# Kernel tuning notes

Hardware: AMD Instinct MI355X
Metric: run time of the kernel (lower is better)

## Reference

```python
import jax, jax.numpy as jnp
import numpy as np

B, HRES, WRES, C, HEADS, WS, SS = 32, 64, 64, 256, 8, 8, 4
N = WS * WS
HID = 4 * C
EPS = 1e-5


def _rel_pos_index(ws):
    coords = np.stack(np.meshgrid(np.arange(ws), np.arange(ws), indexing='ij'))  # [2,ws,ws]
    cf = coords.reshape(2, -1)
    rel = (cf[:, :, None] - cf[:, None, :]).transpose(1, 2, 0)  # [N,N,2]
    rel[:, :, 0] += ws - 1
    rel[:, :, 1] += ws - 1
    rel[:, :, 0] *= 2 * ws - 1
    return rel.sum(-1).reshape(-1)  # [N*N]


def _attn_mask(H, W, ws, ss):
    img = np.zeros((H, W))
    cnt = 0
    for hs in (slice(0, -ws), slice(-ws, -ss), slice(-ss, None)):
        for wsl in (slice(0, -ws), slice(-ws, -ss), slice(-ss, None)):
            img[hs, wsl] = cnt
            cnt += 1
    mw = img.reshape(H // ws, ws, W // ws, ws).transpose(0, 2, 1, 3).reshape(-1, ws * ws)
    am = mw[:, None, :] - mw[:, :, None]  # [nW,N,N]
    return np.where(am != 0, -100.0, 0.0).astype(np.float32)


_RPI = jnp.asarray(_rel_pos_index(WS))
_MASK = jnp.asarray(_attn_mask(HRES, WRES, WS, SS))  # [nW,N,N]


def _ln(x, g, b):
    m = x.mean(-1, keepdims=True)
    v = ((x - m) ** 2).mean(-1, keepdims=True)
    return (x - m) / jnp.sqrt(v + EPS) * g + b


def setup_inputs() -> dict:
    key = jax.random.key(0)
    ks = jax.random.split(key, 16)
    s = 0.02
    return {
        'x': jax.random.normal(ks[0], (B, HRES * WRES, C), jnp.float32),
        'norm1_g': jnp.ones((C,), jnp.float32),
        'norm1_b': jnp.zeros((C,), jnp.float32),
        'qkv_w': jax.random.normal(ks[1], (3 * C, C), jnp.float32) * s,
        'qkv_b': jnp.zeros((3 * C,), jnp.float32),
        'rpb_table': jax.random.normal(ks[2], ((2 * WS - 1) ** 2, HEADS), jnp.float32) * s,
        'proj_w': jax.random.normal(ks[3], (C, C), jnp.float32) * s,
        'proj_b': jnp.zeros((C,), jnp.float32),
        'norm2_g': jnp.ones((C,), jnp.float32),
        'norm2_b': jnp.zeros((C,), jnp.float32),
        'fc1_w': jax.random.normal(ks[4], (HID, C), jnp.float32) * s,
        'fc1_b': jnp.zeros((HID,), jnp.float32),
        'fc2_w': jax.random.normal(ks[5], (C, HID), jnp.float32) * s,
        'fc2_b': jnp.zeros((C,), jnp.float32),
        'H': HRES,
        'W': WRES,
    }


def reference(x, norm1_g, norm1_b, qkv_w, qkv_b, rpb_table, proj_w, proj_b,
              norm2_g, norm2_b, fc1_w, fc1_b, fc2_w, fc2_b, H, W):
    Bn, L, Cd = x.shape
    ws, ss, nh = WS, SS, HEADS
    hd = Cd // nh
    shortcut = x
    h = _ln(x, norm1_g, norm1_b).reshape(Bn, H, W, Cd)
    # cyclic shift (H,W divisible by ws -> no padding needed)
    h = jnp.roll(h, (-ss, -ss), axis=(1, 2))
    # window partition: [B,H,W,C] -> [B*nW, N, C]
    h = h.reshape(Bn, H // ws, ws, W // ws, ws, Cd).transpose(0, 1, 3, 2, 4, 5).reshape(-1, N, Cd)
    qkv = (h @ qkv_w.T + qkv_b).reshape(-1, N, 3, nh, hd).transpose(2, 0, 3, 1, 4)
    q, k, v = qkv[0], qkv[1], qkv[2]  # [B_,h,N,d]
    attn = jnp.einsum('bhnd,bhmd->bhnm', q * (hd ** -0.5), k)
    rpb = rpb_table[_RPI].reshape(N, N, nh).transpose(2, 0, 1)  # [h,N,N]
    attn = attn + rpb[None]
    nW = _MASK.shape[0]
    attn = attn.reshape(Bn, nW, nh, N, N) + _MASK[None, :, None]
    attn = jax.nn.softmax(attn.reshape(-1, nh, N, N), axis=-1)
    o = jnp.einsum('bhnm,bhmd->bhnd', attn, v).transpose(0, 2, 1, 3).reshape(-1, N, Cd)
    o = o @ proj_w.T + proj_b
    # window reverse + reverse shift
    o = o.reshape(Bn, H // ws, W // ws, ws, ws, Cd).transpose(0, 1, 3, 2, 4, 5).reshape(Bn, H, W, Cd)
    o = jnp.roll(o, (ss, ss), axis=(1, 2)).reshape(Bn, L, Cd)
    x = shortcut + o
    h2 = _ln(x, norm2_g, norm2_b)
    h2 = jax.nn.gelu(h2 @ fc1_w.T + fc1_b, approximate=False)
    return x + (h2 @ fc2_w.T + fc2_b)
```

## Files before the change

kernel.cpp:

```cpp
#include <hip/hip_runtime.h>
#include <hip/hip_bf16.h>
#include <stdint.h>

typedef __bf16 bf16_t;
typedef __bf16 bf16x8 __attribute__((ext_vector_type(8)));
typedef __bf16 bf16x4 __attribute__((ext_vector_type(4)));
typedef float f32x4 __attribute__((ext_vector_type(4)));

#define MROWS 131072

__device__ __forceinline__ bf16_t to_bf16(float f) {
  __hip_bfloat16 h = __float2bfloat16(f);
  return *reinterpret_cast<bf16_t*>(&h);
}

__device__ __forceinline__ f32x4 mfma16(bf16x8 a, bf16x8 b, f32x4 c) {
  return __builtin_amdgcn_mfma_f32_16x16x32_bf16(a, b, c, 0, 0, 0);
}

__device__ __forceinline__ void gload16(const void* g, void* l) {
  __builtin_amdgcn_global_load_lds(
      (const __attribute__((address_space(1))) void*)g,
      (__attribute__((address_space(3))) void*)l, 16, 0, 0);
}

__device__ __forceinline__ int map_row(int m) {
  int b   = m >> 12;
  int rem = m & 4095;
  int win = rem >> 6;
  int n   = rem & 63;
  int gh  = ((win >> 3) << 3) + (n >> 3);
  int gw  = ((win & 7) << 3) + (n & 7);
  int sh  = (gh + 4) & 63;
  int sw  = (gw + 4) & 63;
  return (b << 12) + (sh << 6) + sw;
}

__global__ __launch_bounds__(256) void cvt_all(const float* __restrict__ qkv_w,
                                               const float* __restrict__ proj_w,
                                               const float* __restrict__ fc1_w,
                                               const float* __restrict__ fc2_w,
                                               bf16_t* __restrict__ qkv_o,
                                               bf16_t* __restrict__ proj_o,
                                               bf16_t* __restrict__ fc1_o,
                                               bf16_t* __restrict__ fc2_o) {
  int i = blockIdx.x * 256 + threadIdx.x;
  if (i < 196608)       qkv_o[i] = to_bf16(qkv_w[i]);
  else if (i < 262144)  proj_o[i - 196608] = to_bf16(proj_w[i - 196608]);
  else if (i < 524288)  fc1_o[i - 262144] = to_bf16(fc1_w[i - 262144]);
  else                  fc2_o[i - 524288] = to_bf16(fc2_w[i - 524288]);
}

__global__ __launch_bounds__(256) void bias_kernel(const float* __restrict__ rpbt,
                                                   float* __restrict__ bias) {
  int idx = blockIdx.x * 256 + threadIdx.x;
  int m = idx & 63, n = (idx >> 6) & 63, h = (idx >> 12) & 7, c = idx >> 15;
  int yn = n >> 3, xn = n & 7, ym = m >> 3, xm = m & 7;
  float v = rpbt[((yn - ym + 7) * 15 + (xn - xm + 7)) * 8 + h];
  int rn = (c & 2) ? (yn < 4 ? 1 : 2) : 0;
  int cn = (c & 1) ? (xn < 4 ? 1 : 2) : 0;
  int rm = (c & 2) ? (ym < 4 ? 1 : 2) : 0;
  int cm = (c & 1) ? (xm < 4 ? 1 : 2) : 0;
  if (rn * 3 + cn != rm * 3 + cm) v -= 100.0f;
  bias[idx] = v;
}

template <bool PERM>
__global__ __launch_bounds__(256) void ln_kernel(const float* __restrict__ xin,
                                                 const float* __restrict__ g,
                                                 const float* __restrict__ b,
                                                 bf16_t* __restrict__ out) {
  int row  = (blockIdx.x << 2) + (threadIdx.x >> 6);
  int lane = threadIdx.x & 63;
  int src  = PERM ? map_row(row) : row;
  float4 v = *reinterpret_cast<const float4*>(xin + (size_t)src * 256 + (lane << 2));
  float s = v.x + v.y + v.z + v.w;
#pragma unroll
  for (int d = 1; d < 64; d <<= 1) s += __shfl_xor(s, d);
  float mean = s * 0.00390625f;
  float ax = v.x - mean, ay = v.y - mean, az = v.z - mean, aw = v.w - mean;
  float s2 = ax * ax + ay * ay + az * az + aw * aw;
#pragma unroll
  for (int d = 1; d < 64; d <<= 1) s2 += __shfl_xor(s2, d);
  float rstd = rsqrtf(s2 * 0.00390625f + 1e-5f);
  float4 gv = *reinterpret_cast<const float4*>(g + (lane << 2));
  float4 bv = *reinterpret_cast<const float4*>(b + (lane << 2));
  bf16x4 o4;
  o4[0] = to_bf16(ax * rstd * gv.x + bv.x);
  o4[1] = to_bf16(ay * rstd * gv.y + bv.y);
  o4[2] = to_bf16(az * rstd * gv.z + bv.z);
  o4[3] = to_bf16(aw * rstd * gv.w + bv.w);
  *reinterpret_cast<bf16x4*>(out + (size_t)row * 256 + (lane << 2)) = o4;
}

template <int EPI>
__global__ __launch_bounds__(512, 4) void gemm128x256(const bf16_t* __restrict__ A,
                                                      const bf16_t* __restrict__ W,
                                                      const float* __restrict__ bias,
                                                      void* __restrict__ outp,
                                                      void* __restrict__ outp2,
                                                      void* __restrict__ outp3,
                                                      const float* __restrict__ resid,
                                                      const float* __restrict__ n2g,
                                                      const float* __restrict__ n2b,
                                                      bf16_t* __restrict__ x2n,
                                                      int M, int N, int K, int NBN) {
  extern __shared__ __align__(16) char smem[];
  bf16_t* As  = (bf16_t*)smem;
  bf16_t* Bs  = As + 3 * 4096;
  float*  lnS = (float*)(Bs + 3 * 8192);
  float*  lnQ = lnS + 512;
  float*  lnMR = lnQ + 512;
  const int tid  = threadIdx.x;
  const int lane = tid & 63, lo = lane & 15, hi = lane >> 4;
  const int wid  = tid >> 6, wm = wid >> 2, wn = wid & 3;
  const int cpx = gridDim.x >> 3;
  const int wg  = (blockIdx.x & 7) * cpx + (blockIdx.x >> 3);
  const int bn = (wg % NBN) << 8, bm = (wg / NBN) << 7;
  f32x4 acc[4][4] = {};

#define STG(buf, kt)                                                          \
  {                                                                           \
    int k0s = (kt) << 5;                                                      \
    {                                                                         \
      int ch = tid;                                                           \
      int row = ch >> 2, sl = ((ch & 3) ^ ((row >> 1) & 3)) << 3;             \
      gload16(A + (size_t)(bm + row) * K + k0s + sl,                          \
              &As[((buf) << 12) + (ch << 3)]);                                \
    }                                                                         \
    _Pragma("unroll") for (int l = 0; l < 2; ++l) {                           \
      int ch = (l << 9) + tid;                                                \
      int row = ch >> 2, sl = ((ch & 3) ^ ((row >> 1) & 3)) << 3;             \
      gload16(W + (size_t)(bn + row) * K + k0s + sl,                          \
              &Bs[((buf) << 13) + (ch << 3)]);                                \
    }                                                                         \
  }

  const int nt = K >> 5;
  STG(0, 0);
  STG(1, 1);

  int cb = 0;
  for (int t = 0; t < nt; ++t) {
    if (t + 1 < nt) { asm volatile("s_waitcnt vmcnt(3)" ::: "memory"); }
    else            { asm volatile("s_waitcnt vmcnt(0)" ::: "memory"); }
    __builtin_amdgcn_s_barrier();
    if (t + 2 < nt) {
      int sb = (cb == 0) ? 2 : cb - 1;
      STG(sb, t + 2);
    }
    const bf16_t* as = &As[cb << 12];
    const bf16_t* bs = &Bs[cb << 13];
    bf16x8 af[4], bfr[4];
#pragma unroll
    for (int i = 0; i < 4; ++i) {
      int ra = (wm << 6) + (i << 4) + lo;
      af[i] = *reinterpret_cast<const bf16x8*>(&as[ra * 32 + ((hi ^ ((ra >> 1) & 3)) << 3)]);
    }
#pragma unroll
    for (int j = 0; j < 4; ++j) {
      int rb = (wn << 6) + (j << 4) + lo;
      bfr[j] = *reinterpret_cast<const bf16x8*>(&bs[rb * 32 + ((hi ^ ((rb >> 1) & 3)) << 3)]);
    }
    __builtin_amdgcn_s_setprio(1);
#pragma unroll
    for (int i = 0; i < 4; ++i)
#pragma unroll
      for (int j = 0; j < 4; ++j)
        acc[i][j] = mfma16(af[i], bfr[j], acc[i][j]);
    __builtin_amdgcn_s_setprio(0);
    cb = (cb == 2) ? 0 : cb + 1;
  }
#undef STG

  float bv4[4];
#pragma unroll
  for (int nf = 0; nf < 4; ++nf) bv4[nf] = bias[bn + (wn << 6) + (nf << 4) + lo];

  if constexpr (EPI == 2) {
    float* o = (float*)outp;
    float gv[4], bnv[4];
#pragma unroll
    for (int nf = 0; nf < 4; ++nf) {
      int col = (wn << 6) + (nf << 4) + lo;
      gv[nf] = n2g[col]; bnv[nf] = n2b[col];
    }
#pragma unroll
    for (int mf = 0; mf < 4; ++mf)
#pragma unroll
      for (int r = 0; r < 4; ++r) {
        int rl = (wm << 6) + (mf << 4) + (hi << 2) + r;
        int xr = map_row(bm + rl);
        float s = 0.f, q = 0.f;
#pragma unroll
        for (int nf = 0; nf < 4; ++nf) {
          int col = (wn << 6) + (nf << 4) + lo;
          size_t idx = (size_t)xr * 256 + col;
          float v = resid[idx] + acc[mf][nf][r] + bv4[nf];
          acc[mf][nf][r] = v;
          o[idx] = v;
          s += v; q += v * v;
        }
#pragma unroll
        for (int d = 1; d < 16; d <<= 1) { s += __shfl_xor(s, d); q += __shfl_xor(q, d); }
        if (lo == 0) { lnS[(rl << 2) + wn] = s; lnQ[(rl << 2) + wn] = q; }
      }
    __syncthreads();
    if (tid < 128) {
      float s = lnS[tid << 2] + lnS[(tid << 2) + 1] + lnS[(tid << 2) + 2] + lnS[(tid << 2) + 3];
      float q = lnQ[tid << 2] + lnQ[(tid << 2) + 1] + lnQ[(tid << 2) + 2] + lnQ[(tid << 2) + 3];
      float mean = s * 0.00390625f;
      float var  = q * 0.00390625f - mean * mean;
      lnMR[tid << 1] = mean;
      lnMR[(tid << 1) + 1] = rsqrtf(var + 1e-5f);
    }
    __syncthreads();
#pragma unroll
    for (int mf = 0; mf < 4; ++mf)
#pragma unroll
      for (int r = 0; r < 4; ++r) {
        int rl = (wm << 6) + (mf << 4) + (hi << 2) + r;
        int xr = map_row(bm + rl);
        float mean = lnMR[rl << 1], rstd = lnMR[(rl << 1) + 1];
#pragma unroll
        for (int nf = 0; nf < 4; ++nf) {
          int col = (wn << 6) + (nf << 4) + lo;
          x2n[(size_t)xr * 256 + col] = to_bf16((acc[mf][nf][r] - mean) * rstd * gv[nf] + bnv[nf]);
        }
      }
  } else if constexpr (EPI == 4) {
    __syncthreads();
    bf16_t* Os = (bf16_t*)smem;
#pragma unroll
    for (int mf = 0; mf < 4; ++mf)
#pragma unroll
      for (int r = 0; r < 4; ++r) {
        int rl = (wm << 6) + (mf << 4) + (hi << 2) + r;
#pragma unroll
        for (int nf = 0; nf < 4; ++nf) {
          int col = (wn << 6) + (nf << 4) + lo;
          Os[rl * 264 + col] = to_bf16(acc[mf][nf][r] + bv4[nf]);
        }
      }
    __syncthreads();
    {
      bf16_t* base = (bn == 0) ? (bf16_t*)outp
                   : (bn == 256) ? (bf16_t*)outp2 : (bf16_t*)outp3;
      bf16_t* dst = base + ((size_t)wid * MROWS + bm) * 32;
#pragma unroll
      for (int p = 0; p < 8; ++p) {
        int off = (p << 9) + (lane << 3);
        int row = off >> 5, d0 = off & 31;
        bf16x8 v = *reinterpret_cast<const bf16x8*>(&Os[row * 264 + (wid << 5) + d0]);
        *reinterpret_cast<bf16x8*>(dst + off) = v;
      }
    }
  } else {
    __syncthreads();
    bf16_t* Os = (bf16_t*)smem;
#pragma unroll
    for (int mf = 0; mf < 4; ++mf)
#pragma unroll
      for (int r = 0; r < 4; ++r) {
        int rl = (wm << 6) + (mf << 4) + (hi << 2) + r;
#pragma unroll
        for (int nf = 0; nf < 4; ++nf) {
          int col = (wn << 6) + (nf << 4) + lo;
          float v = acc[mf][nf][r] + bv4[nf];
          if constexpr (EPI == 1) v = 0.5f * v * (1.0f + erff(v * 0.70710678118654752f));
          Os[rl * 264 + col] = to_bf16(v);
        }
      }
    __syncthreads();
    {
      bf16_t* o = (bf16_t*)outp;
#pragma unroll
      for (int p = 0; p < 8; ++p) {
        int off = (p << 9) + (lane << 3);
        int row = (wid << 4) + (off >> 8);
        int col = off & 255;
        bf16x8 v = *reinterpret_cast<const bf16x8*>(&Os[row * 264 + col]);
        *reinterpret_cast<bf16x8*>(o + (size_t)(bm + row) * N + bn + col) = v;
      }
    }
  }
}

template <int EPI>
__global__ __launch_bounds__(256) void gemm_bt(const bf16_t* __restrict__ A,
                                               const bf16_t* __restrict__ W,
                                               const float* __restrict__ bias,
                                               void* __restrict__ outp,
                                               int M, int N, int K, int NBN) {
  __shared__ __align__(16) bf16_t As[3 * 128 * 32];
  __shared__ __align__(16) bf16_t Bs[3 * 128 * 32];
  const int tid  = threadIdx.x;
  const int lane = tid & 63, lo = lane & 15, hi = lane >> 4;
  const int wave = tid >> 6;
  const int cpx = gridDim.x >> 3;
  const int wg  = (blockIdx.x & 7) * cpx + (blockIdx.x >> 3);
  const int bn = (wg % NBN) << 7, bm = (wg / NBN) << 7;
  const int wr = (wave >> 1) << 6, wc = (wave & 1) << 6;
  f32x4 acc[4][4] = {};

#define STAGE(buf, kt)                                                         \
  {                                                                            \
    int k0s = (kt) << 5;                                                       \
    _Pragma("unroll") for (int it = 0; it < 2; ++it) {                         \
      int ch = (it << 8) + tid;                                                \
      int r = ch >> 2;                                                         \
      int kf = ((ch & 3) ^ ((r >> 1) & 3)) << 3;                               \
      gload16(A + (size_t)(bm + r) * K + k0s + kf, &As[((buf) << 12) + (ch << 3)]); \
      gload16(W + (size_t)(bn + r) * K + k0s + kf, &Bs[((buf) << 12) + (ch << 3)]); \
    }                                                                          \
  }

  const int nt = K >> 5;
  STAGE(0, 0);
  STAGE(1, 1);

  int cb = 0;
  for (int t = 0; t < nt; ++t) {
    if (t + 1 < nt) { asm volatile("s_waitcnt vmcnt(4)" ::: "memory"); }
    else            { asm volatile("s_waitcnt vmcnt(0)" ::: "memory"); }
    __builtin_amdgcn_s_barrier();
    if (t + 2 < nt) {
      int sb = (cb == 0) ? 2 : cb - 1;
      STAGE(sb, t + 2);
    }
    const bf16_t* as = &As[cb << 12];
    const bf16_t* bs = &Bs[cb << 12];
    bf16x8 af[4], bfr[4];
#pragma unroll
    for (int i = 0; i < 4; ++i) {
      int ra = wr + (i << 4) + lo;
      af[i] = *reinterpret_cast<const bf16x8*>(&as[ra * 32 + ((hi ^ ((ra >> 1) & 3)) << 3)]);
    }
#pragma unroll
    for (int j = 0; j < 4; ++j) {
      int rb = wc + (j << 4) + lo;
      bfr[j] = *reinterpret_cast<const bf16x8*>(&bs[rb * 32 + ((hi ^ ((rb >> 1) & 3)) << 3)]);
    }
    __builtin_amdgcn_s_setprio(1);
#pragma unroll
    for (int i = 0; i < 4; ++i)
#pragma unroll
      for (int j = 0; j < 4; ++j)
        acc[i][j] = mfma16(af[i], bfr[j], acc[i][j]);
    __builtin_amdgcn_s_setprio(0);
    cb = (cb == 2) ? 0 : cb + 1;
  }
#undef STAGE

  float bv[4];
#pragma unroll
  for (int j = 0; j < 4; ++j) bv[j] = bias[bn + wc + (j << 4) + lo];

#pragma unroll
  for (int i = 0; i < 4; ++i)
#pragma unroll
    for (int r = 0; r < 4; ++r) {
      int row = bm + wr + (i << 4) + (hi << 2) + r;
      float* o = (float*)outp;
#pragma unroll
      for (int j = 0; j < 4; ++j) {
        int col = bn + wc + (j << 4) + lo;
        size_t idx = (size_t)row * 256 + col;
        o[idx] = o[idx] + acc[i][j][r] + bv[j];
      }
    }
}

__global__ __launch_bounds__(512) void attn_kernel(const bf16_t* __restrict__ qh,
                                                   const bf16_t* __restrict__ kh,
                                                   const bf16_t* __restrict__ vh,
                                                   const float* __restrict__ bias,
                                                   bf16_t* __restrict__ o) {
  __shared__ __align__(16) bf16_t Pl[4][64 * 72];
  __shared__ __align__(16) bf16_t Vt[4][32 * 72];
  const int tid = threadIdx.x;
  const int lane = tid & 63, lo = lane & 15, hi = lane >> 4;
  const int w = tid >> 6;
  const int wh = w >> 1, sub = w & 1;
  const int id = (blockIdx.x << 2) + wh;
  const int win = id >> 3, h = id & 7;
  const size_t hb = ((size_t)h * MROWS + (size_t)win * 64) * 32;
  const bf16_t* qb = qh + hb;
  const bf16_t* kb = kh + hb;
  const bf16_t* vb = vh + hb;

  {
    int m  = (sub << 5) + (lane & 31);
    int dh = (lane >> 5) << 4;
    const bf16_t* vp = vb + (size_t)m * 32 + dh;
    bf16x8 v0 = *reinterpret_cast<const bf16x8*>(vp);
    bf16x8 v1 = *reinterpret_cast<const bf16x8*>(vp + 8);
#pragma unroll
    for (int e = 0; e < 8; ++e) {
      Vt[wh][(dh + e) * 72 + m]     = v0[e];
      Vt[wh][(dh + 8 + e) * 72 + m] = v1[e];
    }
  }

  bf16x8 qa[2], ka[4];
#pragma unroll
  for (int il = 0; il < 2; ++il)
    qa[il] = *reinterpret_cast<const bf16x8*>(qb + ((sub << 5) + (il << 4) + lo) * 32 + (hi << 3));
#pragma unroll
  for (int j = 0; j < 4; ++j)
    ka[j] = *reinterpret_cast<const bf16x8*>(kb + ((j << 4) + lo) * 32 + (hi << 3));
  f32x4 s4[2][4] = {};
#pragma unroll
  for (int il = 0; il < 2; ++il)
#pragma unroll
    for (int j = 0; j < 4; ++j) s4[il][j] = mfma16(qa[il], ka[j], s4[il][j]);

  const int whw = (win & 63) >> 3, www = win & 7;
  const int cls = ((whw == 7) ? 2 : 0) + ((www == 7) ? 1 : 0);
  const float* bb = bias + ((size_t)cls * 8 + h) * 4096;
  const float scale = 0.17677669529663687f;

  float pinv[2][4];
#pragma unroll
  for (int il = 0; il < 2; ++il) {
#pragma unroll
    for (int r = 0; r < 4; ++r) {
      int n = (sub << 5) + (il << 4) + (hi << 2) + r;
      const float* brow = bb + n * 64 + lo;
      float vals[4], mx = -1e30f;
#pragma unroll
      for (int j = 0; j < 4; ++j) {
        float val = s4[il][j][r] * scale + brow[j << 4];
        vals[j] = val;
        mx = fmaxf(mx, val);
      }
#pragma unroll
      for (int d = 1; d < 16; d <<= 1) mx = fmaxf(mx, __shfl_xor(mx, d));
      float sum = 0.0f;
#pragma unroll
      for (int j = 0; j < 4; ++j) {
        float p = __expf(vals[j] - mx);
        sum += p;
        Pl[wh][n * 72 + (j << 4) + lo] = to_bf16(p);
      }
#pragma unroll
      for (int d = 1; d < 16; d <<= 1) sum += __shfl_xor(sum, d);
      pinv[il][r] = 1.0f / sum;
    }
  }

  __syncthreads();

  f32x4 oa[2][2] = {};
#pragma unroll
  for (int kt = 0; kt < 2; ++kt) {
    bf16x8 pa[2], va[2];
#pragma unroll
    for (int il = 0; il < 2; ++il)
      pa[il] = *reinterpret_cast<const bf16x8*>(&Pl[wh][((sub << 5) + (il << 4) + lo) * 72 + (kt << 5) + (hi << 3)]);
#pragma unroll
    for (int dt = 0; dt < 2; ++dt)
      va[dt] = *reinterpret_cast<const bf16x8*>(&Vt[wh][((dt << 4) + lo) * 72 + (kt << 5) + (hi << 3)]);
#pragma unroll
    for (int il = 0; il < 2; ++il)
#pragma unroll
      for (int dt = 0; dt < 2; ++dt) oa[il][dt] = mfma16(pa[il], va[dt], oa[il][dt]);
  }

  bf16_t* ob = o + (size_t)win * (64 * 256) + h * 32;
#pragma unroll
  for (int il = 0; il < 2; ++il)
#pragma unroll
    for (int r = 0; r < 4; ++r) {
      int n = (sub << 5) + (il << 4) + (hi << 2) + r;
      float piv = pinv[il][r];
#pragma unroll
      for (int dt = 0; dt < 2; ++dt)
        ob[(size_t)n * 256 + (dt << 4) + lo] = to_bf16(oa[il][dt][r] * piv);
    }
}

extern "C" void kernel_launch(void* const* d_in, const int* in_sizes, int n_in,
                              void* d_out, int out_size, void* d_ws, size_t ws_size,
                              hipStream_t stream) {
  const float* x      = (const float*)d_in[0];
  const float* n1g    = (const float*)d_in[1];
  const float* n1b    = (const float*)d_in[2];
  const float* qkv_w  = (const float*)d_in[3];
  const float* qkv_b  = (const float*)d_in[4];
  const float* rpbt   = (const float*)d_in[5];
  const float* proj_w = (const float*)d_in[6];
  const float* proj_b = (const float*)d_in[7];
  const float* n2g    = (const float*)d_in[8];
  const float* n2b    = (const float*)d_in[9];
  const float* fc1_w  = (const float*)d_in[10];
  const float* fc1_b  = (const float*)d_in[11];
  const float* fc2_w  = (const float*)d_in[12];
  const float* fc2_b  = (const float*)d_in[13];
  float* out = (float*)d_out;
  char*  ws  = (char*)d_ws;

  const size_t MB64 = 67108864;
  bf16_t* hln  = (bf16_t*)(ws);
  bf16_t* obuf = (bf16_t*)(ws);
  bf16_t* h2   = (bf16_t*)(ws);
  bf16_t* qbuf = (bf16_t*)(ws + MB64);
  bf16_t* x2n  = (bf16_t*)(ws + MB64);
  bf16_t* wb   = (bf16_t*)(ws + 2 * MB64);
  bf16_t* qkv_wb  = wb;
  bf16_t* proj_wb = qkv_wb + 196608;
  bf16_t* fc1_wb  = proj_wb + 65536;
  bf16_t* fc2_wb  = fc1_wb + 262144;
  float*  biast   = (float*)(fc2_wb + 262144);
  bf16_t* kbuf = (bf16_t*)d_out;
  bf16_t* vbuf = kbuf + 33554432;

  const int SMEM_G = 73728;
  const int SMEM_P = 78848;
  hipFuncSetAttribute(reinterpret_cast<const void*>(gemm128x256<1>),
                      hipFuncAttributeMaxDynamicSharedMemorySize, SMEM_G);
  hipFuncSetAttribute(reinterpret_cast<const void*>(gemm128x256<2>),
                      hipFuncAttributeMaxDynamicSharedMemorySize, SMEM_P);
  hipFuncSetAttribute(reinterpret_cast<const void*>(gemm128x256<4>),
                      hipFuncAttributeMaxDynamicSharedMemorySize, SMEM_G);

  cvt_all<<<3072, 256, 0, stream>>>(qkv_w, proj_w, fc1_w, fc2_w,
                                    qkv_wb, proj_wb, fc1_wb, fc2_wb);
  bias_kernel<<<512, 256, 0, stream>>>(rpbt, biast);

  ln_kernel<true><<<32768, 256, 0, stream>>>(x, n1g, n1b, hln);

  gemm128x256<4><<<3072, 512, SMEM_G, stream>>>(hln, qkv_wb, qkv_b, qbuf, kbuf, vbuf,
                                                nullptr, nullptr, nullptr, nullptr,
                                                MROWS, 768, 256, 3);

  attn_kernel<<<4096, 512, 0, stream>>>(qbuf, kbuf, vbuf, biast, obuf);

  gemm128x256<2><<<1024, 512, SMEM_P, stream>>>(obuf, proj_wb, proj_b, out, nullptr, nullptr,
                                                x, n2g, n2b, x2n, MROWS, 256, 256, 1);

  for (int c = 0; c < 4; ++c) {
    const bf16_t* xa = x2n + (size_t)c * 32768 * 256;
    gemm128x256<1><<<1024, 512, SMEM_G, stream>>>(xa, fc1_wb, fc1_b, h2, nullptr, nullptr,
                                                  nullptr, nullptr, nullptr, nullptr,
                                                  32768, 1024, 256, 4);
    gemm_bt<3><<<512, 256, 0, stream>>>(h2, fc2_wb, fc2_b, out + (size_t)c * 32768 * 256,
                                        32768, 256, 1024, 2);
  }
}
```

Measured before the change: 590.8 us.

## Cut GEMM LDS to double buffer and split epilogue staging to raise occupancy

The GEMM moves from a triple-buffered LDS pipeline to a double buffer with two barriers per K step. The epilogue now stages 64-row halves through LDS in two passes, which shrinks shared memory from 72KB to 48KB so more workgroups can reside per CU, and launch bounds rise to 6 waves. The attention kernel's P tile row stride drops from 72 to 68 elements to save LDS, also with a higher launch-bounds hint. The risks are less latency hiding from prefetching only one stage ahead, extra barriers, and possible register spills under the tighter bounds.

```diff
diff --git a/kernel.cpp b/kernel.cpp
--- a/kernel.cpp
+++ b/kernel.cpp
@@ -94,7 +94,7 @@
 }
 
 template <int EPI>
-__global__ __launch_bounds__(512, 4) void gemm128x256(const bf16_t* __restrict__ A,
+__global__ __launch_bounds__(512, 6) void gemm128x256(const bf16_t* __restrict__ A,
                                                       const bf16_t* __restrict__ W,
                                                       const float* __restrict__ bias,
                                                       void* __restrict__ outp,
@@ -107,8 +107,8 @@
                                                       int M, int N, int K, int NBN) {
   extern __shared__ __align__(16) char smem[];
   bf16_t* As  = (bf16_t*)smem;
-  bf16_t* Bs  = As + 3 * 4096;
-  float*  lnS = (float*)(Bs + 3 * 8192);
+  bf16_t* Bs  = As + 2 * 4096;
+  float*  lnS = (float*)(Bs + 2 * 8192);
   float*  lnQ = lnS + 512;
   float*  lnMR = lnQ + 512;
   const int tid  = threadIdx.x;
@@ -139,18 +139,13 @@
   const int nt = K >> 5;
   STG(0, 0);
   STG(1, 1);
-
-  int cb = 0;
+  asm volatile("s_waitcnt vmcnt(3)" ::: "memory");
+  __builtin_amdgcn_s_barrier();
+
   for (int t = 0; t < nt; ++t) {
-    if (t + 1 < nt) { asm volatile("s_waitcnt vmcnt(3)" ::: "memory"); }
-    else            { asm volatile("s_waitcnt vmcnt(0)" ::: "memory"); }
-    __builtin_amdgcn_s_barrier();
-    if (t + 2 < nt) {
-      int sb = (cb == 0) ? 2 : cb - 1;
-      STG(sb, t + 2);
-    }
-    const bf16_t* as = &As[cb << 12];
-    const bf16_t* bs = &Bs[cb << 13];
+    const int cur = t & 1;
+    const bf16_t* as = &As[cur << 12];
+    const bf16_t* bs = &Bs[cur << 13];
     bf16x8 af[4], bfr[4];
 #pragma unroll
     for (int i = 0; i < 4; ++i) {
@@ -169,7 +164,16 @@
       for (int j = 0; j < 4; ++j)
         acc[i][j] = mfma16(af[i], bfr[j], acc[i][j]);
     __builtin_amdgcn_s_setprio(0);
-    cb = (cb == 2) ? 0 : cb + 1;
+    if (t + 1 < nt) {
+      __builtin_amdgcn_s_barrier();
+      if (t + 2 < nt) {
+        STG(cur, t + 2);
+        asm volatile("s_waitcnt vmcnt(3)" ::: "memory");
+      } else {
+        asm volatile("s_waitcnt vmcnt(0)" ::: "memory");
+      }
+      __builtin_amdgcn_s_barrier();
+    }
   }
 #undef STG
 
@@ -229,58 +233,64 @@
         }
       }
   } else if constexpr (EPI == 4) {
-    __syncthreads();
+    bf16_t* base = (bn == 0) ? (bf16_t*)outp
+                 : (bn == 256) ? (bf16_t*)outp2 : (bf16_t*)outp3;
     bf16_t* Os = (bf16_t*)smem;
 #pragma unroll
-    for (int mf = 0; mf < 4; ++mf)
-#pragma unroll
-      for (int r = 0; r < 4; ++r) {
-        int rl = (wm << 6) + (mf << 4) + (hi << 2) + r;
-#pragma unroll
-        for (int nf = 0; nf < 4; ++nf) {
-          int col = (wn << 6) + (nf << 4) + lo;
-          Os[rl * 264 + col] = to_bf16(acc[mf][nf][r] + bv4[nf]);
-        }
-      }
-    __syncthreads();
-    {
-      bf16_t* base = (bn == 0) ? (bf16_t*)outp
-                   : (bn == 256) ? (bf16_t*)outp2 : (bf16_t*)outp3;
-      bf16_t* dst = base + ((size_t)wid * MROWS + bm) * 32;
-#pragma unroll
-      for (int p = 0; p < 8; ++p) {
+    for (int pass = 0; pass < 2; ++pass) {
+      __syncthreads();
+      if (wm == pass) {
+#pragma unroll
+        for (int mf = 0; mf < 4; ++mf)
+#pragma unroll
+          for (int r = 0; r < 4; ++r) {
+            int rl = (mf << 4) + (hi << 2) + r;
+#pragma unroll
+            for (int nf = 0; nf < 4; ++nf) {
+              int col = (wn << 6) + (nf << 4) + lo;
+              Os[rl * 264 + col] = to_bf16(acc[mf][nf][r] + bv4[nf]);
+            }
+          }
+      }
+      __syncthreads();
+      bf16_t* dst = base + ((size_t)wid * MROWS + bm + (pass << 6)) * 32;
+#pragma unroll
+      for (int p = 0; p < 4; ++p) {
         int off = (p << 9) + (lane << 3);
         int row = off >> 5, d0 = off & 31;
-        bf16x8 v = *reinterpret_cast<const bf16x8*>(&Os[row * 264 + (wid << 5) + d0]);
-        *reinterpret_cast<bf16x8*>(dst + off) = v;
+        bf16x8 vv = *reinterpret_cast<const bf16x8*>(&Os[row * 264 + (wid << 5) + d0]);
+        *reinterpret_cast<bf16x8*>(dst + off) = vv;
       }
     }
   } else {
-    __syncthreads();
+    bf16_t* o = (bf16_t*)outp;
     bf16_t* Os = (bf16_t*)smem;
 #pragma unroll
-    for (int mf = 0; mf < 4; ++mf)
-#pragma unroll
-      for (int r = 0; r < 4; ++r) {
-        int rl = (wm << 6) + (mf << 4) + (hi << 2) + r;
-#pragma unroll
-        for (int nf = 0; nf < 4; ++nf) {
-          int col = (wn << 6) + (nf << 4) + lo;
-          float v = acc[mf][nf][r] + bv4[nf];
-          if constexpr (EPI == 1) v = 0.5f * v * (1.0f + erff(v * 0.70710678118654752f));
-          Os[rl * 264 + col] = to_bf16(v);
-        }
-      }
-    __syncthreads();
-    {
-      bf16_t* o = (bf16_t*)outp;
-#pragma unroll
-      for (int p = 0; p < 8; ++p) {
+    for (int pass = 0; pass < 2; ++pass) {
+      __syncthreads();
+      if (wm == pass) {
+#pragma unroll
+        for (int mf = 0; mf < 4; ++mf)
+#pragma unroll
+          for (int r = 0; r < 4; ++r) {
+            int rl = (mf << 4) + (hi << 2) + r;
+#pragma unroll
+            for (int nf = 0; nf < 4; ++nf) {
+              int col = (wn << 6) + (nf << 4) + lo;
+              float v = acc[mf][nf][r] + bv4[nf];
+              if constexpr (EPI == 1) v = 0.5f * v * (1.0f + erff(v * 0.70710678118654752f));
+              Os[rl * 264 + col] = to_bf16(v);
+            }
+          }
+      }
+      __syncthreads();
+#pragma unroll
+      for (int p = 0; p < 4; ++p) {
         int off = (p << 9) + (lane << 3);
-        int row = (wid << 4) + (off >> 8);
+        int row = (wid << 3) + (off >> 8);
         int col = off & 255;
-        bf16x8 v = *reinterpret_cast<const bf16x8*>(&Os[row * 264 + col]);
-        *reinterpret_cast<bf16x8*>(o + (size_t)(bm + row) * N + bn + col) = v;
+        bf16x8 vv = *reinterpret_cast<const bf16x8*>(&Os[row * 264 + col]);
+        *reinterpret_cast<bf16x8*>(o + (size_t)(bm + (pass << 6) + row) * N + bn + col) = vv;
       }
     }
   }
@@ -371,12 +381,12 @@
     }
 }
 
-__global__ __launch_bounds__(512) void attn_kernel(const bf16_t* __restrict__ qh,
-                                                   const bf16_t* __restrict__ kh,
-                                                   const bf16_t* __restrict__ vh,
-                                                   const float* __restrict__ bias,
-                                                   bf16_t* __restrict__ o) {
-  __shared__ __align__(16) bf16_t Pl[4][64 * 72];
+__global__ __launch_bounds__(512, 6) void attn_kernel(const bf16_t* __restrict__ qh,
+                                                      const bf16_t* __restrict__ kh,
+                                                      const bf16_t* __restrict__ vh,
+                                                      const float* __restrict__ bias,
+                                                      bf16_t* __restrict__ o) {
+  __shared__ __align__(16) bf16_t Pl[4][64 * 68];
   __shared__ __align__(16) bf16_t Vt[4][32 * 72];
   const int tid = threadIdx.x;
   const int lane = tid & 63, lo = lane & 15, hi = lane >> 4;
@@ -441,7 +451,7 @@
       for (int j = 0; j < 4; ++j) {
         float p = __expf(vals[j] - mx);
         sum += p;
-        Pl[wh][n * 72 + (j << 4) + lo] = to_bf16(p);
+        Pl[wh][n * 68 + (j << 4) + lo] = to_bf16(p);
       }
 #pragma unroll
       for (int d = 1; d < 16; d <<= 1) sum += __shfl_xor(sum, d);
@@ -457,7 +467,7 @@
     bf16x8 pa[2], va[2];
 #pragma unroll
     for (int il = 0; il < 2; ++il)
-      pa[il] = *reinterpret_cast<const bf16x8*>(&Pl[wh][((sub << 5) + (il << 4) + lo) * 72 + (kt << 5) + (hi << 3)]);
+      pa[il] = *reinterpret_cast<const bf16x8*>(&Pl[wh][((sub << 5) + (il << 4) + lo) * 68 + (kt << 5) + (hi << 3)]);
 #pragma unroll
     for (int dt = 0; dt < 2; ++dt)
       va[dt] = *reinterpret_cast<const bf16x8*>(&Vt[wh][((dt << 4) + lo) * 72 + (kt << 5) + (hi << 3)]);
@@ -515,8 +525,8 @@
   bf16_t* kbuf = (bf16_t*)d_out;
   bf16_t* vbuf = kbuf + 33554432;
 
-  const int SMEM_G = 73728;
-  const int SMEM_P = 78848;
+  const int SMEM_G = 49152;
+  const int SMEM_P = 54272;
   hipFuncSetAttribute(reinterpret_cast<const void*>(gemm128x256<1>),
                       hipFuncAttributeMaxDynamicSharedMemorySize, SMEM_G);
   hipFuncSetAttribute(reinterpret_cast<const void*>(gemm128x256<2>),
```

Measured after the change: 1.839 ms. 211% more time.
